# Performance work log

Hardware: AMD Instinct MI355X
Metric: run time of the kernel (lower is better)

## Reference

```python
import jax, jax.numpy as jnp
import numpy as np
from jax import lax

TAU = 30.0  # softmax temperature


def setup_inputs() -> dict:
    key = jax.random.key(0)
    ks = jax.random.split(key, 6)
    N, Ci, Co, H, K, KW = 16, 64, 64, 256, 3, 4
    x = jax.random.normal(ks[0], (N, Ci, H, H), jnp.float32)
    # bank of KW candidate kernels: (Co, KW, Ci, K, K), kaiming-ish scale
    w_bank = jax.random.normal(ks[1], (Co, KW, Ci, K, K), jnp.float32) * (2.0 / (Co * K * K)) ** 0.5
    b_bank = jax.random.normal(ks[2], (Co, KW), jnp.float32) * 0.01
    # attention MLP (two 1x1 convs): Ci -> Ci//KW -> KW
    att_w1 = jax.random.normal(ks[3], (Ci // KW, Ci), jnp.float32) * (1.0 / Ci) ** 0.5
    att_b1 = jnp.zeros((Ci // KW,), jnp.float32)
    att_w2 = jax.random.normal(ks[4], (KW, Ci // KW), jnp.float32) * (KW / Ci) ** 0.5
    att_b2 = jnp.zeros((KW,), jnp.float32)
    return {"x": x, "w_bank": w_bank, "b_bank": b_bank,
            "att_w1": att_w1, "att_b1": att_b1, "att_w2": att_w2, "att_b2": att_b2}


def reference(x, w_bank, b_bank, att_w1, att_b1, att_w2, att_b2):
    # attention over weight banks: 1x1 conv -> ReLU -> 1x1 conv -> global avg pool -> softmax(/tau)
    h = jax.nn.relu(jnp.einsum('nchw,dc->ndhw', x, att_w1) + att_b1[None, :, None, None])
    logits = jnp.einsum('ndhw,ed->nehw', h, att_w2) + att_b2[None, :, None, None]
    pooled = jnp.mean(logits, axis=(2, 3))          # [N, KW] (avg_pool2d with kernel=H on square input)
    pi = jax.nn.softmax(pooled / TAU, axis=1)       # [N, KW]
    # per-sample aggregated kernels/biases
    w = jnp.einsum('okcij,nk->nocij', w_bank, pi)   # [N, Co, Ci, K, K]
    b = jnp.einsum('ok,nk->no', b_bank, pi)         # [N, Co]
    # per-sample conv (equivalent to the groups=N conv2d trick)
    def conv_one(xi, wi):
        return lax.conv_general_dilated(xi[None], wi, window_strides=(1, 1),
                                        padding=[(1, 1), (1, 1)],
                                        dimension_numbers=('NCHW', 'OIHW', 'NCHW'))[0]
    y = jax.vmap(conv_one)(x, w)                    # [N, Co, H, W]
    return y + b[:, :, None, None]
```

## Files before the change

### kernel.cpp

```cpp
#include <hip/hip_runtime.h>
#include <hip/hip_bf16.h>

typedef short short8 __attribute__((ext_vector_type(8)));
typedef float f32x4 __attribute__((ext_vector_type(4)));
typedef unsigned short ushort_t;

#define AS1 __attribute__((address_space(1)))
#define AS3 __attribute__((address_space(3)))

__device__ __forceinline__ ushort_t f2bf(float f) {
    unsigned u = __builtin_bit_cast(unsigned, f);
    unsigned r = (u + 0x7FFFu + ((u >> 16) & 1u)) >> 16;
    return (ushort_t)r;
}

__device__ __forceinline__ void gload_lds16(const void* g, void* l) {
    __builtin_amdgcn_global_load_lds((const AS1 unsigned*)g, (AS3 unsigned*)l, 16, 0, 0);
}

__global__ __launch_bounds__(256) void dc_k0_zeroborder(ushort_t* __restrict__ x_t)
{
    const int b = blockIdx.x, t = threadIdx.x;
    const int n = b >> 1, row = (b & 1) ? 257 : 0;
    short8 z = {0, 0, 0, 0, 0, 0, 0, 0};
    short8* p = reinterpret_cast<short8*>(x_t + (size_t)(n * 258 + row) * 258 * 64);
    for (int i = t; i < 2064; i += 256) p[i] = z;
}

__global__ __launch_bounds__(256) void dc_k1_stage_attn(
    const float* __restrict__ x, const float* __restrict__ w1,
    const float* __restrict__ b1, float* __restrict__ s_glob,
    ushort_t* __restrict__ x_t)
{
    __shared__ unsigned xt32[256 * 32];
    __shared__ ushort_t w1s[16 * 64];
    __shared__ float sacc[16];

    const int n = blockIdx.y, h = blockIdx.x, t = threadIdx.x;
    if (t < 16) sacc[t] = 0.f;
#pragma unroll
    for (int q = 0; q < 4; ++q) { int idx = q * 256 + t; w1s[idx] = f2bf(w1[idx]); }

    const float* xr = x + ((size_t)n * 64) * 65536 + (size_t)h * 256;
    const int sw = (t & 7) << 2;
    for (int cp = 0; cp < 32; ++cp) {
        float a = xr[(size_t)(2 * cp) * 65536 + t];
        float b = xr[(size_t)(2 * cp + 1) * 65536 + t];
        xt32[(t * 32 + cp) ^ sw] = (unsigned)f2bf(a) | ((unsigned)f2bf(b) << 16);
    }
    __syncthreads();

    const int lane = t & 63, wv = t >> 6, l15 = lane & 15, lg = lane >> 4;
    const short8* xt8 = reinterpret_cast<const short8*>(xt32);
    const short8* w18 = reinterpret_cast<const short8*>(w1s);

    short8 a0 = w18[l15 * 8 + lg];
    short8 a1 = w18[l15 * 8 + 4 + lg];
    float b1v[4];
#pragma unroll
    for (int r = 0; r < 4; ++r) b1v[r] = b1[lg * 4 + r];

    float rs[4] = {0.f, 0.f, 0.f, 0.f};
#pragma unroll
    for (int q = 0; q < 4; ++q) {
        int px = (wv * 4 + q) * 16 + l15;
        int pb = px * 8, ps = px & 7;
        short8 bb0 = xt8[pb + (lg ^ ps)];
        short8 bb1 = xt8[pb + ((4 + lg) ^ ps)];
        f32x4 hacc = {0.f, 0.f, 0.f, 0.f};
        hacc = __builtin_amdgcn_mfma_f32_16x16x32_bf16(a0, bb0, hacc, 0, 0, 0);
        hacc = __builtin_amdgcn_mfma_f32_16x16x32_bf16(a1, bb1, hacc, 0, 0, 0);
#pragma unroll
        for (int r = 0; r < 4; ++r) rs[r] += fmaxf(hacc[r] + b1v[r], 0.f);
    }
#pragma unroll
    for (int off = 1; off < 16; off <<= 1)
#pragma unroll
        for (int r = 0; r < 4; ++r) rs[r] += __shfl_xor(rs[r], off);
    if (l15 == 0) {
#pragma unroll
        for (int r = 0; r < 4; ++r) atomicAdd(&sacc[lg * 4 + r], rs[r]);
    }
    __syncthreads();
    if (t < 16) atomicAdd(&s_glob[n * 16 + t], sacc[t]);

    ushort_t* xo = x_t + (((size_t)n * 258 + h + 1) * 258 + 1) * 64;
    const int cb = t & 7, pxr = t >> 3;
#pragma unroll
    for (int rr = 0; rr < 8; ++rr) {
        int px = rr * 32 + pxr;
        short8 v = xt8[px * 8 + (cb ^ (px & 7))];
        *reinterpret_cast<short8*>(xo + (size_t)px * 64 + cb * 8) = v;
    }
    if (t < 16) {
        short8 z = {0, 0, 0, 0, 0, 0, 0, 0};
        size_t colbase = (((size_t)n * 258 + h + 1) * 258 + ((t < 8) ? 0 : 257)) * 64;
        reinterpret_cast<short8*>(x_t + colbase)[t & 7] = z;
    }
}

__global__ void dc_k2a_softmax_bias(
    const float* __restrict__ s_glob, const float* __restrict__ w2,
    const float* __restrict__ b2, const float* __restrict__ b_bank,
    float* __restrict__ pi, float* __restrict__ b_agg)
{
    __shared__ float piL[16][4];
    const int t = threadIdx.x;
    if (t < 16) {
        int n = t;
        float z[4];
#pragma unroll
        for (int e = 0; e < 4; ++e) {
            float p = 0.f;
            for (int d = 0; d < 16; ++d) p += w2[e * 16 + d] * s_glob[n * 16 + d];
            z[e] = (b2[e] + p * (1.f / 65536.f)) * (1.f / 30.f);
        }
        float m = fmaxf(fmaxf(z[0], z[1]), fmaxf(z[2], z[3]));
        float ex[4], sum = 0.f;
#pragma unroll
        for (int e = 0; e < 4; ++e) { ex[e] = expf(z[e] - m); sum += ex[e]; }
        float inv = 1.f / sum;
#pragma unroll
        for (int e = 0; e < 4; ++e) { float v = ex[e] * inv; pi[n * 4 + e] = v; piL[n][e] = v; }
    }
    __syncthreads();
    for (int r = 0; r < 16; ++r) {
        float v = 0.f;
#pragma unroll
        for (int kw = 0; kw < 4; ++kw) v += piL[r][kw] * b_bank[t * 4 + kw];
        b_agg[r * 64 + t] = v;
    }
}

__global__ void dc_k2b_aggw(const float* __restrict__ w_bank,
                            const float* __restrict__ pi,
                            ushort_t* __restrict__ A_frag)
{
    __shared__ float lw[2304];
    const int o = blockIdx.x, n = blockIdx.y, t = threadIdx.x;
    const float* wrow = w_bank + (size_t)o * 2304;
    for (int rr = 0; rr < 36; ++rr) lw[rr * 64 + t] = wrow[rr * 64 + t];
    float p0 = pi[n * 4 + 0], p1 = pi[n * 4 + 1], p2 = pi[n * 4 + 2], p3 = pi[n * 4 + 3];
    __syncthreads();
    const int c = t;
    const int cc = c >> 5, lg = (c >> 3) & 3, e = c & 7;
    const int mf = o >> 4, l15 = o & 15;
    ushort_t* base = A_frag + (size_t)n * 18 * 4 * 64 * 8;
#pragma unroll
    for (int ij = 0; ij < 9; ++ij) {
        float v = p0 * lw[0 * 576 + c * 9 + ij] + p1 * lw[1 * 576 + c * 9 + ij]
                + p2 * lw[2 * 576 + c * 9 + ij] + p3 * lw[3 * 576 + c * 9 + ij];
        int ks = ij * 2 + cc;
        base[(((ks * 4 + mf) * 64) + (lg * 16 + l15)) * 8 + e] = f2bf(v);
    }
}

__global__ __launch_bounds__(256, 1) void dc_k3_conv(
    const ushort_t* __restrict__ x_t, const ushort_t* __restrict__ A_frag,
    const float* __restrict__ b_agg, float* __restrict__ out)
{
    __shared__ char lds[73728 + 4 * 17408];
    char* ldsA = lds;
    char* ldsW = lds + 73728;

    int bid = blockIdx.x;
    int nb = (bid & 7) * 32 + (bid >> 3);
    const int n = nb >> 4;
    const int half = nb & 1;
    const int strip = (nb >> 1) & 7;
    const int h0 = strip * 32;
    const int w0 = half << 7;

    const int t = threadIdx.x, lane = t & 63, wv = t >> 6;
    const int l15 = lane & 15, lg = lane >> 4;
    const int pxl = wv * 32;

    const char* srcb = (const char*)x_t;
    const char* Asrc = (const char*)A_frag + (size_t)n * 73728;

    for (int q = 0; q < 18; ++q) {
        int j = wv * 18 + q;
        gload_lds16(Asrc + j * 1024 + lane * 16, ldsA + j * 1024);
    }
    for (int r = 0; r < 3; ++r) {
        size_t rowoff = ((size_t)(n * 258 + h0 + r) * 258 + w0) * 128;
        for (int k = wv; k < 17; k += 4) {
            unsigned q = k * 1024 + lane * 16;
            unsigned so = q ^ (((q >> 7) & 7) << 4);
            gload_lds16(srcb + rowoff + so, ldsW + r * 17408 + k * 1024);
        }
    }
    asm volatile("s_waitcnt vmcnt(0)" ::: "memory");
    __builtin_amdgcn_s_barrier();
    __builtin_amdgcn_sched_barrier(0);

    int boff[3][2][2];
#pragma unroll
    for (int kj = 0; kj < 3; ++kj)
#pragma unroll
        for (int cc = 0; cc < 2; ++cc)
#pragma unroll
            for (int nf = 0; nf < 2; ++nf) {
                int colL = pxl + nf * 16 + l15 + kj;
                boff[kj][cc][nf] = (colL * 128 + cc * 64 + lg * 16)
                                   ^ ((colL & 7) << 4);
            }
    const int aoff = lane * 16;

    const float* bn = b_agg + n * 64;
    float bv[4][4];
#pragma unroll
    for (int mf = 0; mf < 4; ++mf)
#pragma unroll
        for (int r = 0; r < 4; ++r) bv[mf][r] = bn[mf * 16 + lg * 4 + r];

#pragma unroll 1
    for (int i = 0; i < 32; ++i) {
        if (i <= 30) {
            size_t rowoff = ((size_t)(n * 258 + h0 + i + 3) * 258 + w0) * 128;
            char* dst = ldsW + ((i + 3) & 3) * 17408;
            for (int k = wv; k < 17; k += 4) {
                unsigned q = k * 1024 + lane * 16;
                unsigned so = q ^ (((q >> 7) & 7) << 4);
                gload_lds16(srcb + rowoff + so, dst + k * 1024);
            }
        }
        __builtin_amdgcn_sched_barrier(0);

        const char* sbs[3] = { ldsW + ((i) & 3) * 17408,
                               ldsW + ((i + 1) & 3) * 17408,
                               ldsW + ((i + 2) & 3) * 17408 };
        f32x4 acc[4][2] = {};
        short8 afb[2][4], bfb[2][2];
#pragma unroll
        for (int mf = 0; mf < 4; ++mf)
            afb[0][mf] = *reinterpret_cast<const short8*>(ldsA + mf * 1024 + aoff);
#pragma unroll
        for (int nf = 0; nf < 2; ++nf)
            bfb[0][nf] = *reinterpret_cast<const short8*>(sbs[0] + boff[0][0][nf]);

#pragma unroll
        for (int ks = 0; ks < 18; ++ks) {
            const int cur = ks & 1, nxt = cur ^ 1;
            if (ks < 17) {
                const int k1 = ks + 1;
                const int ki1 = k1 / 6, r1 = k1 % 6;
                const int kj1 = r1 >> 1, cc1 = r1 & 1;
#pragma unroll
                for (int mf = 0; mf < 4; ++mf)
                    afb[nxt][mf] = *reinterpret_cast<const short8*>(
                        ldsA + (k1 * 4 + mf) * 1024 + aoff);
#pragma unroll
                for (int nf = 0; nf < 2; ++nf)
                    bfb[nxt][nf] = *reinterpret_cast<const short8*>(
                        sbs[ki1] + boff[kj1][cc1][nf]);
            }
#pragma unroll
            for (int mf = 0; mf < 4; ++mf)
#pragma unroll
                for (int nf = 0; nf < 2; ++nf)
                    acc[mf][nf] = __builtin_amdgcn_mfma_f32_16x16x32_bf16(
                        afb[cur][mf], bfb[cur][nf], acc[mf][nf], 0, 0, 0);
        }

        const int h = h0 + i;
#pragma unroll
        for (int mf = 0; mf < 4; ++mf)
#pragma unroll
            for (int nf = 0; nf < 2; ++nf) {
                const int col = w0 + pxl + nf * 16 + l15;
#pragma unroll
                for (int r = 0; r < 4; ++r)
                    out[((size_t)(n * 64 + mf * 16 + lg * 4 + r) << 16)
                        + (size_t)h * 256 + col] = acc[mf][nf][r] + bv[mf][r];
            }

        asm volatile("s_waitcnt vmcnt(16)" ::: "memory");
        __builtin_amdgcn_s_barrier();
        __builtin_amdgcn_sched_barrier(0);
    }
}

extern "C" void kernel_launch(void* const* d_in, const int* in_sizes, int n_in,
                              void* d_out, int out_size, void* d_ws, size_t ws_size,
                              hipStream_t stream) {
    const float* x      = (const float*)d_in[0];
    const float* w_bank = (const float*)d_in[1];
    const float* b_bank = (const float*)d_in[2];
    const float* att_w1 = (const float*)d_in[3];
    const float* att_b1 = (const float*)d_in[4];
    const float* att_w2 = (const float*)d_in[5];
    const float* att_b2 = (const float*)d_in[6];
    float* out = (float*)d_out;

    char* ws = (char*)d_ws;
    float*    s_glob = (float*)ws;
    float*    pi     = (float*)(ws + 1024);
    float*    b_agg  = (float*)(ws + 2048);
    ushort_t* A_frag = (ushort_t*)(ws + 8192);
    ushort_t* x_t    = (ushort_t*)(ws + (2ull << 20));

    hipMemsetAsync(s_glob, 0, 16 * 16 * sizeof(float), stream);

    dc_k0_zeroborder<<<32, 256, 0, stream>>>(x_t);
    dc_k1_stage_attn<<<dim3(256, 16), 256, 0, stream>>>(x, att_w1, att_b1, s_glob, x_t);
    dc_k2a_softmax_bias<<<1, 64, 0, stream>>>(s_glob, att_w2, att_b2, b_bank, pi, b_agg);
    dc_k2b_aggw<<<dim3(64, 16), 64, 0, stream>>>(w_bank, pi, A_frag);
    dc_k3_conv<<<256, 256, 0, stream>>>(x_t, A_frag, b_agg, out);
}
```

Measured before the change: 202.9 us.

## Compute two output rows per iteration to reuse A fragments across rows

The conv main loop now produces two output rows per iteration, so each A-weight fragment loaded from LDS feeds twice as many MFMAs. The input ring buffer grows from 4 to 5 row slots, and the staging of the two next rows is split, with the second issued mid-loop after a barrier. This cuts LDS reads of weights and the count of barriers per row. In exchange it doubles the accumulator registers, adds LDS use, and replaces the partial vmcnt wait with a full drain before the stores.

```diff
diff --git a/kernel.cpp b/kernel.cpp
--- a/kernel.cpp
+++ b/kernel.cpp
@@ -159,7 +159,7 @@
     const ushort_t* __restrict__ x_t, const ushort_t* __restrict__ A_frag,
     const float* __restrict__ b_agg, float* __restrict__ out)
 {
-    __shared__ char lds[73728 + 4 * 17408];
+    __shared__ char lds[73728 + 5 * 17408];
     char* ldsA = lds;
     char* ldsW = lds + 73728;
 
@@ -178,18 +178,21 @@
     const char* srcb = (const char*)x_t;
     const char* Asrc = (const char*)A_frag + (size_t)n * 73728;
 
+    auto stage_row = [&](int rr, int slot) {
+        size_t rowoff = ((size_t)(n * 258 + h0 + rr) * 258 + w0) * 128;
+        char* dst = ldsW + slot * 17408;
+        for (int k = wv; k < 17; k += 4) {
+            unsigned q = k * 1024 + lane * 16;
+            unsigned so = q ^ (((q >> 7) & 7) << 4);
+            gload_lds16(srcb + rowoff + so, dst + k * 1024);
+        }
+    };
+
     for (int q = 0; q < 18; ++q) {
         int j = wv * 18 + q;
         gload_lds16(Asrc + j * 1024 + lane * 16, ldsA + j * 1024);
     }
-    for (int r = 0; r < 3; ++r) {
-        size_t rowoff = ((size_t)(n * 258 + h0 + r) * 258 + w0) * 128;
-        for (int k = wv; k < 17; k += 4) {
-            unsigned q = k * 1024 + lane * 16;
-            unsigned so = q ^ (((q >> 7) & 7) << 4);
-            gload_lds16(srcb + rowoff + so, ldsW + r * 17408 + k * 1024);
-        }
-    }
+    for (int r = 0; r < 4; ++r) stage_row(r, r);
     asm volatile("s_waitcnt vmcnt(0)" ::: "memory");
     __builtin_amdgcn_s_barrier();
     __builtin_amdgcn_sched_barrier(0);
@@ -215,69 +218,81 @@
         for (int r = 0; r < 4; ++r) bv[mf][r] = bn[mf * 16 + lg * 4 + r];
 
 #pragma unroll 1
-    for (int i = 0; i < 32; ++i) {
-        if (i <= 30) {
-            size_t rowoff = ((size_t)(n * 258 + h0 + i + 3) * 258 + w0) * 128;
-            char* dst = ldsW + ((i + 3) & 3) * 17408;
-            for (int k = wv; k < 17; k += 4) {
-                unsigned q = k * 1024 + lane * 16;
-                unsigned so = q ^ (((q >> 7) & 7) << 4);
-                gload_lds16(srcb + rowoff + so, dst + k * 1024);
-            }
-        }
+    for (int j = 0; j < 16; ++j) {
+        const int r0 = 2 * j;
+        const int r4 = r0 + 4, r5 = r0 + 5;
+
+        if (r4 <= 33) stage_row(r4, r4 % 5);
         __builtin_amdgcn_sched_barrier(0);
 
-        const char* sbs[3] = { ldsW + ((i) & 3) * 17408,
-                               ldsW + ((i + 1) & 3) * 17408,
-                               ldsW + ((i + 2) & 3) * 17408 };
-        f32x4 acc[4][2] = {};
-        short8 afb[2][4], bfb[2][2];
+        const char* sb[4] = { ldsW + (r0 % 5) * 17408,
+                              ldsW + ((r0 + 1) % 5) * 17408,
+                              ldsW + ((r0 + 2) % 5) * 17408,
+                              ldsW + ((r0 + 3) % 5) * 17408 };
+
+        f32x4 acc[4][2][2] = {};
+        short8 afb[2][4], bfb[2][2][2];
+
 #pragma unroll
         for (int mf = 0; mf < 4; ++mf)
             afb[0][mf] = *reinterpret_cast<const short8*>(ldsA + mf * 1024 + aoff);
 #pragma unroll
-        for (int nf = 0; nf < 2; ++nf)
-            bfb[0][nf] = *reinterpret_cast<const short8*>(sbs[0] + boff[0][0][nf]);
+        for (int o = 0; o < 2; ++o)
+#pragma unroll
+            for (int nf = 0; nf < 2; ++nf)
+                bfb[0][o][nf] = *reinterpret_cast<const short8*>(sb[o] + boff[0][0][nf]);
 
 #pragma unroll
         for (int ks = 0; ks < 18; ++ks) {
+            if (ks == 6) {
+                __builtin_amdgcn_s_barrier();
+                if (r5 <= 33) stage_row(r5, r0 % 5);
+                __builtin_amdgcn_sched_barrier(0);
+            }
             const int cur = ks & 1, nxt = cur ^ 1;
             if (ks < 17) {
                 const int k1 = ks + 1;
-                const int ki1 = k1 / 6, r1 = k1 % 6;
-                const int kj1 = r1 >> 1, cc1 = r1 & 1;
+                const int ki1 = k1 / 6, rem = k1 % 6;
+                const int kj1 = rem >> 1, cc1 = rem & 1;
 #pragma unroll
                 for (int mf = 0; mf < 4; ++mf)
                     afb[nxt][mf] = *reinterpret_cast<const short8*>(
                         ldsA + (k1 * 4 + mf) * 1024 + aoff);
 #pragma unroll
+                for (int o = 0; o < 2; ++o)
+#pragma unroll
+                    for (int nf = 0; nf < 2; ++nf)
+                        bfb[nxt][o][nf] = *reinterpret_cast<const short8*>(
+                            sb[ki1 + o] + boff[kj1][cc1][nf]);
+            }
+#pragma unroll
+            for (int mf = 0; mf < 4; ++mf)
+#pragma unroll
                 for (int nf = 0; nf < 2; ++nf)
-                    bfb[nxt][nf] = *reinterpret_cast<const short8*>(
-                        sbs[ki1] + boff[kj1][cc1][nf]);
-            }
+#pragma unroll
+                    for (int o = 0; o < 2; ++o)
+                        acc[mf][nf][o] = __builtin_amdgcn_mfma_f32_16x16x32_bf16(
+                            afb[cur][mf], bfb[cur][o][nf], acc[mf][nf][o], 0, 0, 0);
+        }
+
+        asm volatile("s_waitcnt vmcnt(0)" ::: "memory");
+        __builtin_amdgcn_sched_barrier(0);
+#pragma unroll
+        for (int o = 0; o < 2; ++o) {
+            const int h = h0 + r0 + o;
 #pragma unroll
             for (int mf = 0; mf < 4; ++mf)
 #pragma unroll
-                for (int nf = 0; nf < 2; ++nf)
-                    acc[mf][nf] = __builtin_amdgcn_mfma_f32_16x16x32_bf16(
-                        afb[cur][mf], bfb[cur][nf], acc[mf][nf], 0, 0, 0);
+                for (int nf = 0; nf < 2; ++nf) {
+                    const int col = w0 + pxl + nf * 16 + l15;
+#pragma unroll
+                    for (int r = 0; r < 4; ++r)
+                        out[((size_t)(n * 64 + mf * 16 + lg * 4 + r) << 16)
+                            + (size_t)h * 256 + col] = acc[mf][nf][o][r] + bv[mf][r];
+                }
         }
-
-        const int h = h0 + i;
-#pragma unroll
-        for (int mf = 0; mf < 4; ++mf)
-#pragma unroll
-            for (int nf = 0; nf < 2; ++nf) {
-                const int col = w0 + pxl + nf * 16 + l15;
-#pragma unroll
-                for (int r = 0; r < 4; ++r)
-                    out[((size_t)(n * 64 + mf * 16 + lg * 4 + r) << 16)
-                        + (size_t)h * 256 + col] = acc[mf][nf][r] + bv[mf][r];
-            }
-
-        asm volatile("s_waitcnt vmcnt(16)" ::: "memory");
+        __builtin_amdgcn_sched_barrier(0);
         __builtin_amdgcn_s_barrier();
-        __builtin_amdgcn_sched_barrier(0);
     }
 }
 
```

New measurement: 197.5 us. -2.7%, faster.
